# Performance work log

Hardware: AMD Instinct MI355X
Metric: run time of the kernel (lower is better)

The kernel has to match this reference:

```python
import jax, jax.numpy as jnp
import numpy as np

TEMP = 0.07
BASE_TEMP = 0.07
NUM_CLASSES = 1000


def setup_inputs() -> dict:
    key = jax.random.key(0)
    k1, k2, k3, k4 = jax.random.split(key, 4)
    B, V, D, Q = 1024, 2, 128, 65536
    features = jax.random.normal(k1, (B, V, D), jnp.float32)
    features = features / jnp.linalg.norm(features, axis=-1, keepdims=True)
    labels = jax.random.randint(k2, (B,), 0, NUM_CLASSES)
    queue = jax.random.normal(k3, (Q, D), jnp.float32)
    queue = queue / jnp.linalg.norm(queue, axis=-1, keepdims=True)
    queue_labels = jax.random.randint(k4, (Q,), 0, NUM_CLASSES)
    return {"features": features, "labels": labels, "queue": queue, "queue_labels": queue_labels}


def reference(features, labels, queue, queue_labels):
    # features: [B, 2, D]; queue: [Q, D]; labels: [B]; queue_labels: [Q]
    B = features.shape[0]
    f1 = features[:, 0]  # view 1 -> enqueued at the front of the queue
    f2 = features[:, 1]  # view 2 -> anchor
    queue_new = jnp.concatenate([f1, queue[:-B]], axis=0)            # [Q, D]
    qlab_new = jnp.concatenate([labels, queue_labels[:-B]], axis=0)  # [Q]

    # anchor_dot_contrast: [B, Q]
    logits = jnp.matmul(f2, queue_new.T) / TEMP
    logits = logits - jax.lax.stop_gradient(jnp.max(logits, axis=1, keepdims=True))

    rows = jnp.arange(B)
    # scatter(ones, 1, arange(B).view(-1,1), 0): zero at (i, i) -> excludes own enqueued view
    self_mask = jnp.ones(logits.shape, logits.dtype).at[rows, rows].set(0.0)
    pos_mask = (labels[:, None] == qlab_new[None, :]).astype(logits.dtype)  # [B, Q]
    neg_mask = jnp.square(pos_mask - 1.0)  # 1 where different class (pre self-mask), else 0
    pos_mask = pos_mask * self_mask

    e = jnp.exp(logits)
    # supervised term: denominator over negatives only
    log_prob = logits - jnp.log(jnp.sum(e * neg_mask, axis=1, keepdims=True))
    mean_log_prob_pos = jnp.sum(pos_mask * log_prob, axis=1) / jnp.sum(pos_mask, axis=1)

    # triplet/self term: denominator over everything except the self column
    log_self_diff = logits - jnp.log(jnp.sum(e * self_mask, axis=1, keepdims=True))
    triplet = log_self_diff[rows, rows]  # sim_mask selects the paired-view column (i, i)

    scale = TEMP / BASE_TEMP
    loss = jnp.mean(-scale * (triplet + mean_log_prob_pos) / 2.0)
    self_loss = jnp.mean(-scale * triplet)
    class_loss = jnp.mean(-scale * mean_log_prob_pos)
    return (loss, self_loss, class_loss)
```

## Files before the change

kernel.cpp:

```cpp
#include <hip/hip_runtime.h>
#include <math.h>

#define BB 1024
#define DD 128
#define QQ 65536
#define CHUNK 32
#define THREADS 256
#define COLS_PER_BLOCK 128
#define F2G (BB / COLS_PER_BLOCK)
#define NSLICES 256
#define INV_T 14.285714285714286f
#define SCALE 20.609929155556627f
#define LN2F 0.6931471805599453f

typedef short short8 __attribute__((ext_vector_type(8)));
typedef float f32x4  __attribute__((ext_vector_type(4)));
typedef unsigned short us4 __attribute__((ext_vector_type(4)));

#if __has_builtin(__builtin_amdgcn_exp2f)
#define EXP2F(x) __builtin_amdgcn_exp2f(x)
#else
#define EXP2F(x) exp2f(x)
#endif

static __device__ __forceinline__ unsigned short bf16rne(float f) {
    union { float f; unsigned u; } v; v.f = f;
    unsigned r = (v.u + 0x7FFFu + ((v.u >> 16) & 1u)) >> 16;
    return (unsigned short)r;
}

static __device__ __forceinline__ short8 pack8s(float4 x, float4 y) {
    short8 r;
    r[0]=(short)bf16rne(x.x*SCALE); r[1]=(short)bf16rne(x.y*SCALE);
    r[2]=(short)bf16rne(x.z*SCALE); r[3]=(short)bf16rne(x.w*SCALE);
    r[4]=(short)bf16rne(y.x*SCALE); r[5]=(short)bf16rne(y.y*SCALE);
    r[6]=(short)bf16rne(y.z*SCALE); r[7]=(short)bf16rne(y.w*SCALE);
    return r;
}
static __device__ __forceinline__ short8 pack8(float4 x, float4 y) {
    short8 r;
    r[0]=(short)bf16rne(x.x); r[1]=(short)bf16rne(x.y);
    r[2]=(short)bf16rne(x.z); r[3]=(short)bf16rne(x.w);
    r[4]=(short)bf16rne(y.x); r[5]=(short)bf16rne(y.y);
    r[6]=(short)bf16rne(y.z); r[7]=(short)bf16rne(y.w);
    return r;
}

template<int PREK>
__global__ __launch_bounds__(256)
void k1_conv(const float* __restrict__ features, const int* __restrict__ labels,
             const float* __restrict__ queue, const int* __restrict__ queue_labels,
             unsigned short* __restrict__ qbf, int* __restrict__ qlabn,
             unsigned short* __restrict__ f2bf, float* __restrict__ srr)
{
    const int blk = blockIdx.x;
    const int t = blk * 256 + threadIdx.x;
    if (PREK && blk < 512) {
        if (blk < 256)
            qlabn[t] = (t < BB) ? labels[t] : queue_labels[t - BB];
#pragma unroll
        for (int k = 0; k < 16; ++k) {
            int u = k * 131072 + t;
            int e = u * 4;
            int row = e >> 7;
            const float* src = (row < BB) ? (features + (size_t)row * 2 * DD + (e & 127))
                                          : (queue + ((size_t)e - (size_t)BB * DD));
            float4 v = *reinterpret_cast<const float4*>(src);
            us4 pk;
            pk[0] = bf16rne(v.x); pk[1] = bf16rne(v.y);
            pk[2] = bf16rne(v.z); pk[3] = bf16rne(v.w);
            *reinterpret_cast<us4*>(qbf + (size_t)e) = pk;
        }
    } else {
        int r = (PREK ? (blk - 512) : blk) * 256 + threadIdx.x;
        const float* f2p = features + (size_t)r * 2 * DD + DD;
        const float* f1p = features + (size_t)r * 2 * DD;
        float d = 0.f;
#pragma unroll
        for (int k = 0; k < DD / 8; ++k) {
            float4 a0 = reinterpret_cast<const float4*>(f2p)[2 * k];
            float4 a1 = reinterpret_cast<const float4*>(f2p)[2 * k + 1];
            float4 b0 = reinterpret_cast<const float4*>(f1p)[2 * k];
            float4 b1 = reinterpret_cast<const float4*>(f1p)[2 * k + 1];
            d += a0.x * b0.x + a0.y * b0.y + a0.z * b0.z + a0.w * b0.w;
            d += a1.x * b1.x + a1.y * b1.y + a1.z * b1.z + a1.w * b1.w;
            if (PREK)
                *reinterpret_cast<short8*>(f2bf + (size_t)r * DD + k * 8) = pack8s(a0, a1);
        }
        srr[r] = d;
    }
}

template<int PRE>
__global__ __launch_bounds__(THREADS)
void supcon_main(const float* __restrict__ features, const int* __restrict__ labels,
                 const float* __restrict__ queue, const int* __restrict__ queue_labels,
                 const unsigned short* __restrict__ qbf, const int* __restrict__ qlabn,
                 const unsigned short* __restrict__ f2bf,
                 float* __restrict__ stats, int nslices)
{
    __shared__ int4 ldsbuf[2][512];

    const int tid = threadIdx.x;
    const int l = tid & 63, w = tid >> 6;
    const int bid = blockIdx.x;
    const int slice = bid % nslices, f2g = bid / nslices;
    const int sliceRows = QQ / nslices;
    const int nchunks = sliceRows / CHUNK;
    const int colbase = f2g * COLS_PER_BLOCK + w * 32;

    short8 bf[2][4];
    int mylab[2];
#pragma unroll
    for (int b = 0; b < 2; ++b) {
        int r = colbase + b * 16 + (l & 15);
        mylab[b] = labels[r];
        if (PRE) {
            const unsigned short* fp = f2bf + (size_t)r * DD + ((l >> 4) * 8);
#pragma unroll
            for (int kk = 0; kk < 4; ++kk)
                bf[b][kk] = *reinterpret_cast<const short8*>(fp + kk * 32);
        } else {
            const float* fp = features + (size_t)r * 2 * DD + DD + ((l >> 4) * 8);
#pragma unroll
            for (int kk = 0; kk < 4; ++kk) {
                float4 x = *reinterpret_cast<const float4*>(fp + kk * 32);
                float4 y = *reinterpret_cast<const float4*>(fp + kk * 32 + 4);
                bf[b][kk] = pack8s(x, y);
            }
        }
    }

    float tot[2]  = {0.f,0.f};
    float pose[2] = {0.f,0.f};
    float psum[2] = {0.f,0.f};
    float npos[2] = {0.f,0.f};

    const int srow = tid >> 3, sseg = tid & 7;
    const int swzs = (srow & 7) << 4;
    const int j0base = slice * sliceRows;

    {
        int j = j0base + srow;
        char* base = (char*)&ldsbuf[0][0] + srow * 256;
        int cb0 = (sseg * 32) ^ swzs;
        if (PRE) {
            const short8* src = reinterpret_cast<const short8*>(
                qbf + (size_t)j * DD + sseg * 16);
            *reinterpret_cast<short8*>(base + cb0)        = src[0];
            *reinterpret_cast<short8*>(base + (cb0 ^ 16)) = src[1];
        } else {
            const float* src = ((j < BB) ? (features + (size_t)j * 2 * DD)
                                         : (queue + (size_t)(j - BB) * DD)) + sseg * 16;
            float4 p0 = reinterpret_cast<const float4*>(src)[0];
            float4 p1 = reinterpret_cast<const float4*>(src)[1];
            float4 p2 = reinterpret_cast<const float4*>(src)[2];
            float4 p3 = reinterpret_cast<const float4*>(src)[3];
            *reinterpret_cast<short8*>(base + cb0)        = pack8(p0, p1);
            *reinterpret_cast<short8*>(base + (cb0 ^ 16)) = pack8(p2, p3);
        }
    }

    int cur = 0;
    for (int c = 0; c < nchunks; ++c) {
        __syncthreads();
        const int cj0 = j0base + c * CHUNK;
        const bool havenext = (c + 1 < nchunks);

        short8 nlo, nhi;
        float4 p0, p1, p2, p3;
        if (havenext) {
            int j = cj0 + CHUNK + srow;
            if (PRE) {
                const short8* src = reinterpret_cast<const short8*>(
                    qbf + (size_t)j * DD + sseg * 16);
                nlo = src[0]; nhi = src[1];
            } else {
                const float* src = ((j < BB) ? (features + (size_t)j * 2 * DD)
                                             : (queue + (size_t)(j - BB) * DD)) + sseg * 16;
                p0 = reinterpret_cast<const float4*>(src)[0];
                p1 = reinterpret_cast<const float4*>(src)[1];
                p2 = reinterpret_cast<const float4*>(src)[2];
                p3 = reinterpret_cast<const float4*>(src)[3];
            }
        }

        const char* abase = (const char*)&ldsbuf[cur][0];
#pragma unroll
        for (int t2 = 0; t2 < 2; ++t2) {
            const int row = t2 * 16 + (l & 15);
            const char* rbase = abase + row * 256;
            const int g16 = (l >> 4) * 16;
            const int swz = (row & 7) << 4;
            const int j0 = cj0 + t2 * 16 + ((l >> 4) << 2);

            int4 ql4;
            if (PRE) ql4 = *reinterpret_cast<const int4*>(qlabn + j0);
            else ql4 = (j0 < BB) ? *reinterpret_cast<const int4*>(labels + j0)
                                 : *reinterpret_cast<const int4*>(queue_labels + (j0 - BB));
            const int* ql = reinterpret_cast<const int*>(&ql4);

            f32x4 acc[2];
#pragma unroll
            for (int b = 0; b < 2; ++b) acc[b] = f32x4{0.f,0.f,0.f,0.f};
#pragma unroll
            for (int kk = 0; kk < 4; ++kk) {
                short8 a = *reinterpret_cast<const short8*>(rbase + ((kk * 64 + g16) ^ swz));
#pragma unroll
                for (int b = 0; b < 2; ++b)
                    acc[b] = __builtin_amdgcn_mfma_f32_16x16x32_bf16(a, bf[b][kk], acc[b], 0, 0, 0);
            }
#pragma unroll
            for (int b = 0; b < 2; ++b) {
#pragma unroll
                for (int reg = 0; reg < 4; ++reg) {
                    float a = acc[b][reg];
                    float e = EXP2F(a);
                    float pf = (ql[reg] == mylab[b]) ? 1.0f : 0.0f;
                    tot[b]  += e;
                    pose[b]  = fmaf(pf, e, pose[b]);
                    psum[b]  = fmaf(pf, a, psum[b]);
                    npos[b] += pf;
                }
            }
        }

        if (havenext) {
            char* base = (char*)&ldsbuf[cur ^ 1][0] + srow * 256;
            int cb0 = (sseg * 32) ^ swzs;
            if (PRE) {
                *reinterpret_cast<short8*>(base + cb0)        = nlo;
                *reinterpret_cast<short8*>(base + (cb0 ^ 16)) = nhi;
            } else {
                *reinterpret_cast<short8*>(base + cb0)        = pack8(p0, p1);
                *reinterpret_cast<short8*>(base + (cb0 ^ 16)) = pack8(p2, p3);
            }
            cur ^= 1;
        }
    }

#pragma unroll
    for (int b = 0; b < 2; ++b) {
#pragma unroll
        for (int off = 16; off <= 32; off <<= 1) {
            tot[b]  += __shfl_xor(tot[b],  off);
            pose[b] += __shfl_xor(pose[b], off);
            psum[b] += __shfl_xor(psum[b], off);
            npos[b] += __shfl_xor(npos[b], off);
        }
    }
    if ((l >> 4) == 0) {
#pragma unroll
        for (int b = 0; b < 2; ++b) {
            float4 v; v.x = tot[b]; v.y = pose[b]; v.z = psum[b]; v.w = npos[b];
            *reinterpret_cast<float4*>(
                stats + ((size_t)(colbase + b * 16 + l) * nslices + slice) * 4) = v;
        }
    }
}

__global__ __launch_bounds__(256)
void f1_rows(const float* __restrict__ stats, const float* __restrict__ srr,
             float* __restrict__ partials, int nslices)
{
    __shared__ float red[4][2];
    int wv = threadIdx.x >> 6, lane = threadIdx.x & 63;
    int r = blockIdx.x * 4 + wv;
    float tot = 0.f, pose = 0.f, ps = 0.f, np = 0.f;
    for (int s = lane; s < nslices; s += 64) {
        float4 v = reinterpret_cast<const float4*>(stats)[(size_t)r * nslices + s];
        tot += v.x; pose += v.y; ps += v.z; np += v.w;
    }
#pragma unroll
    for (int off = 32; off > 0; off >>= 1) {
        tot  += __shfl_xor(tot,  off);
        pose += __shfl_xor(pose, off);
        ps   += __shfl_xor(ps,   off);
        np   += __shfl_xor(np,   off);
    }
    if (lane == 0) {
        float neg  = tot - pose;
        float srow = srr[r] * INV_T;
        float trip = srow - logf(tot - expf(srow));
        float w    = 1.f / (np - 1.f);
        float mlpp = (ps * LN2F - srow) * w - logf(neg);
        red[wv][0] = trip; red[wv][1] = mlpp;
    }
    __syncthreads();
    if (threadIdx.x == 0) {
        partials[blockIdx.x * 2]     = red[0][0] + red[1][0] + red[2][0] + red[3][0];
        partials[blockIdx.x * 2 + 1] = red[0][1] + red[1][1] + red[2][1] + red[3][1];
    }
}

__global__ __launch_bounds__(256)
void f2_out(const float* __restrict__ partials, float* __restrict__ out)
{
    __shared__ float red[4][2];
    int wv = threadIdx.x >> 6, lane = threadIdx.x & 63;
    float2 v = reinterpret_cast<const float2*>(partials)[threadIdx.x];
    float a = v.x, b = v.y;
#pragma unroll
    for (int off = 32; off > 0; off >>= 1) {
        a += __shfl_xor(a, off);
        b += __shfl_xor(b, off);
    }
    if (lane == 0) { red[wv][0] = a; red[wv][1] = b; }
    __syncthreads();
    if (threadIdx.x == 0) {
        float aT = red[0][0] + red[1][0] + red[2][0] + red[3][0];
        float aM = red[0][1] + red[1][1] + red[2][1] + red[3][1];
        float selfl  = -aT / (float)BB;
        float classl = -aM / (float)BB;
        out[0] = 0.5f * (selfl + classl);
        out[1] = selfl;
        out[2] = classl;
    }
}

extern "C" void kernel_launch(void* const* d_in, const int* in_sizes, int n_in,
                              void* d_out, int out_size, void* d_ws, size_t ws_size,
                              hipStream_t stream)
{
    const float* features     = (const float*)d_in[0];
    const int*   labels       = (const int*)  d_in[1];
    const float* queue        = (const float*)d_in[2];
    const int*   queue_labels = (const int*)  d_in[3];
    char* ws = (char*)d_ws;

    const size_t qbf_sz      = (size_t)QQ * DD * 2;
    const size_t f2bf_sz     = (size_t)BB * DD * 2;
    const size_t qlabn_sz    = (size_t)QQ * 4;
    const size_t srr_sz      = 4096;
    const size_t partials_sz = 2048;

    int nslices = NSLICES;
    size_t stats_sz = (size_t)BB * nslices * 16;
    bool pre = ws_size >= qbf_sz + f2bf_sz + qlabn_sz + stats_sz + srr_sz + partials_sz;
    if (!pre) {
        while ((size_t)BB * nslices * 16 + srr_sz + partials_sz > ws_size && nslices > 8)
            nslices >>= 1;
        stats_sz = (size_t)BB * nslices * 16;
    }

    size_t off = 0;
    unsigned short* qbf = nullptr; unsigned short* f2bf = nullptr; int* qlabn = nullptr;
    if (pre) {
        qbf   = (unsigned short*)(ws + off); off += qbf_sz;
        f2bf  = (unsigned short*)(ws + off); off += f2bf_sz;
        qlabn = (int*)(ws + off);            off += qlabn_sz;
    }
    float* stats    = (float*)(ws + off); off += stats_sz;
    float* srr      = (float*)(ws + off); off += srr_sz;
    float* partials = (float*)(ws + off); off += partials_sz;

    if (pre) {
        k1_conv<1><<<dim3(516), dim3(256), 0, stream>>>(
            features, labels, queue, queue_labels, qbf, qlabn, f2bf, srr);
        supcon_main<1><<<dim3(F2G * nslices), dim3(THREADS), 0, stream>>>(
            features, labels, queue, queue_labels, qbf, qlabn, f2bf, stats, nslices);
    } else {
        k1_conv<0><<<dim3(4), dim3(256), 0, stream>>>(
            features, labels, queue, queue_labels, nullptr, nullptr, nullptr, srr);
        supcon_main<0><<<dim3(F2G * nslices), dim3(THREADS), 0, stream>>>(
            features, labels, queue, queue_labels, nullptr, nullptr, nullptr, stats, nslices);
    }

    f1_rows<<<dim3(BB / 4), dim3(256), 0, stream>>>(stats, srr, partials, nslices);
    f2_out<<<dim3(1), dim3(256), 0, stream>>>(partials, (float*)d_out);
}
```

Measured before the change: 63.29 us.

## Drop bf16 pre-conversion kernel and convert fp32 inputs on the fly

Removes the k1_conv pre-pass that converted the whole queue to bf16 in workspace along with the pre-scaled f2 copy and the concatenated labels. The main kernel now always reads fp32 features and queue and packs them to bf16 inline while staging into LDS. The self-similarity dot product moves into f1_rows. This saves one launch and a 16MB bf16 write, but the main kernel now reads twice the bytes per queue row (fp32 instead of bf16) and the f2 bf16 packing is redone in every block.

```diff
diff --git a/kernel.cpp b/kernel.cpp
--- a/kernel.cpp
+++ b/kernel.cpp
@@ -15,7 +15,6 @@
 
 typedef short short8 __attribute__((ext_vector_type(8)));
 typedef float f32x4  __attribute__((ext_vector_type(4)));
-typedef unsigned short us4 __attribute__((ext_vector_type(4)));
 
 #if __has_builtin(__builtin_amdgcn_exp2f)
 #define EXP2F(x) __builtin_amdgcn_exp2f(x)
@@ -46,57 +45,9 @@
     return r;
 }
 
-template<int PREK>
-__global__ __launch_bounds__(256)
-void k1_conv(const float* __restrict__ features, const int* __restrict__ labels,
-             const float* __restrict__ queue, const int* __restrict__ queue_labels,
-             unsigned short* __restrict__ qbf, int* __restrict__ qlabn,
-             unsigned short* __restrict__ f2bf, float* __restrict__ srr)
-{
-    const int blk = blockIdx.x;
-    const int t = blk * 256 + threadIdx.x;
-    if (PREK && blk < 512) {
-        if (blk < 256)
-            qlabn[t] = (t < BB) ? labels[t] : queue_labels[t - BB];
-#pragma unroll
-        for (int k = 0; k < 16; ++k) {
-            int u = k * 131072 + t;
-            int e = u * 4;
-            int row = e >> 7;
-            const float* src = (row < BB) ? (features + (size_t)row * 2 * DD + (e & 127))
-                                          : (queue + ((size_t)e - (size_t)BB * DD));
-            float4 v = *reinterpret_cast<const float4*>(src);
-            us4 pk;
-            pk[0] = bf16rne(v.x); pk[1] = bf16rne(v.y);
-            pk[2] = bf16rne(v.z); pk[3] = bf16rne(v.w);
-            *reinterpret_cast<us4*>(qbf + (size_t)e) = pk;
-        }
-    } else {
-        int r = (PREK ? (blk - 512) : blk) * 256 + threadIdx.x;
-        const float* f2p = features + (size_t)r * 2 * DD + DD;
-        const float* f1p = features + (size_t)r * 2 * DD;
-        float d = 0.f;
-#pragma unroll
-        for (int k = 0; k < DD / 8; ++k) {
-            float4 a0 = reinterpret_cast<const float4*>(f2p)[2 * k];
-            float4 a1 = reinterpret_cast<const float4*>(f2p)[2 * k + 1];
-            float4 b0 = reinterpret_cast<const float4*>(f1p)[2 * k];
-            float4 b1 = reinterpret_cast<const float4*>(f1p)[2 * k + 1];
-            d += a0.x * b0.x + a0.y * b0.y + a0.z * b0.z + a0.w * b0.w;
-            d += a1.x * b1.x + a1.y * b1.y + a1.z * b1.z + a1.w * b1.w;
-            if (PREK)
-                *reinterpret_cast<short8*>(f2bf + (size_t)r * DD + k * 8) = pack8s(a0, a1);
-        }
-        srr[r] = d;
-    }
-}
-
-template<int PRE>
 __global__ __launch_bounds__(THREADS)
 void supcon_main(const float* __restrict__ features, const int* __restrict__ labels,
                  const float* __restrict__ queue, const int* __restrict__ queue_labels,
-                 const unsigned short* __restrict__ qbf, const int* __restrict__ qlabn,
-                 const unsigned short* __restrict__ f2bf,
                  float* __restrict__ stats, int nslices)
 {
     __shared__ int4 ldsbuf[2][512];
@@ -115,19 +66,12 @@
     for (int b = 0; b < 2; ++b) {
         int r = colbase + b * 16 + (l & 15);
         mylab[b] = labels[r];
-        if (PRE) {
-            const unsigned short* fp = f2bf + (size_t)r * DD + ((l >> 4) * 8);
-#pragma unroll
-            for (int kk = 0; kk < 4; ++kk)
-                bf[b][kk] = *reinterpret_cast<const short8*>(fp + kk * 32);
-        } else {
-            const float* fp = features + (size_t)r * 2 * DD + DD + ((l >> 4) * 8);
-#pragma unroll
-            for (int kk = 0; kk < 4; ++kk) {
-                float4 x = *reinterpret_cast<const float4*>(fp + kk * 32);
-                float4 y = *reinterpret_cast<const float4*>(fp + kk * 32 + 4);
-                bf[b][kk] = pack8s(x, y);
-            }
+        const float* fp = features + (size_t)r * 2 * DD + DD + ((l >> 4) * 8);
+#pragma unroll
+        for (int kk = 0; kk < 4; ++kk) {
+            float4 x = *reinterpret_cast<const float4*>(fp + kk * 32);
+            float4 y = *reinterpret_cast<const float4*>(fp + kk * 32 + 4);
+            bf[b][kk] = pack8s(x, y);
         }
     }
 
@@ -142,23 +86,16 @@
 
     {
         int j = j0base + srow;
+        const float* src = ((j < BB) ? (features + (size_t)j * 2 * DD)
+                                     : (queue + (size_t)(j - BB) * DD)) + sseg * 16;
+        float4 p0 = reinterpret_cast<const float4*>(src)[0];
+        float4 p1 = reinterpret_cast<const float4*>(src)[1];
+        float4 p2 = reinterpret_cast<const float4*>(src)[2];
+        float4 p3 = reinterpret_cast<const float4*>(src)[3];
         char* base = (char*)&ldsbuf[0][0] + srow * 256;
         int cb0 = (sseg * 32) ^ swzs;
-        if (PRE) {
-            const short8* src = reinterpret_cast<const short8*>(
-                qbf + (size_t)j * DD + sseg * 16);
-            *reinterpret_cast<short8*>(base + cb0)        = src[0];
-            *reinterpret_cast<short8*>(base + (cb0 ^ 16)) = src[1];
-        } else {
-            const float* src = ((j < BB) ? (features + (size_t)j * 2 * DD)
-                                         : (queue + (size_t)(j - BB) * DD)) + sseg * 16;
-            float4 p0 = reinterpret_cast<const float4*>(src)[0];
-            float4 p1 = reinterpret_cast<const float4*>(src)[1];
-            float4 p2 = reinterpret_cast<const float4*>(src)[2];
-            float4 p3 = reinterpret_cast<const float4*>(src)[3];
-            *reinterpret_cast<short8*>(base + cb0)        = pack8(p0, p1);
-            *reinterpret_cast<short8*>(base + (cb0 ^ 16)) = pack8(p2, p3);
-        }
+        *reinterpret_cast<short8*>(base + cb0)        = pack8(p0, p1);
+        *reinterpret_cast<short8*>(base + (cb0 ^ 16)) = pack8(p2, p3);
     }
 
     int cur = 0;
@@ -167,22 +104,15 @@
         const int cj0 = j0base + c * CHUNK;
         const bool havenext = (c + 1 < nchunks);
 
-        short8 nlo, nhi;
         float4 p0, p1, p2, p3;
         if (havenext) {
             int j = cj0 + CHUNK + srow;
-            if (PRE) {
-                const short8* src = reinterpret_cast<const short8*>(
-                    qbf + (size_t)j * DD + sseg * 16);
-                nlo = src[0]; nhi = src[1];
-            } else {
-                const float* src = ((j < BB) ? (features + (size_t)j * 2 * DD)
-                                             : (queue + (size_t)(j - BB) * DD)) + sseg * 16;
-                p0 = reinterpret_cast<const float4*>(src)[0];
-                p1 = reinterpret_cast<const float4*>(src)[1];
-                p2 = reinterpret_cast<const float4*>(src)[2];
-                p3 = reinterpret_cast<const float4*>(src)[3];
-            }
+            const float* src = ((j < BB) ? (features + (size_t)j * 2 * DD)
+                                         : (queue + (size_t)(j - BB) * DD)) + sseg * 16;
+            p0 = reinterpret_cast<const float4*>(src)[0];
+            p1 = reinterpret_cast<const float4*>(src)[1];
+            p2 = reinterpret_cast<const float4*>(src)[2];
+            p3 = reinterpret_cast<const float4*>(src)[3];
         }
 
         const char* abase = (const char*)&ldsbuf[cur][0];
@@ -194,9 +124,7 @@
             const int swz = (row & 7) << 4;
             const int j0 = cj0 + t2 * 16 + ((l >> 4) << 2);
 
-            int4 ql4;
-            if (PRE) ql4 = *reinterpret_cast<const int4*>(qlabn + j0);
-            else ql4 = (j0 < BB) ? *reinterpret_cast<const int4*>(labels + j0)
+            int4 ql4 = (j0 < BB) ? *reinterpret_cast<const int4*>(labels + j0)
                                  : *reinterpret_cast<const int4*>(queue_labels + (j0 - BB));
             const int* ql = reinterpret_cast<const int*>(&ql4);
 
@@ -228,13 +156,8 @@
         if (havenext) {
             char* base = (char*)&ldsbuf[cur ^ 1][0] + srow * 256;
             int cb0 = (sseg * 32) ^ swzs;
-            if (PRE) {
-                *reinterpret_cast<short8*>(base + cb0)        = nlo;
-                *reinterpret_cast<short8*>(base + (cb0 ^ 16)) = nhi;
-            } else {
-                *reinterpret_cast<short8*>(base + cb0)        = pack8(p0, p1);
-                *reinterpret_cast<short8*>(base + (cb0 ^ 16)) = pack8(p2, p3);
-            }
+            *reinterpret_cast<short8*>(base + cb0)        = pack8(p0, p1);
+            *reinterpret_cast<short8*>(base + (cb0 ^ 16)) = pack8(p2, p3);
             cur ^= 1;
         }
     }
@@ -260,7 +183,7 @@
 }
 
 __global__ __launch_bounds__(256)
-void f1_rows(const float* __restrict__ stats, const float* __restrict__ srr,
+void f1_rows(const float* __restrict__ stats, const float* __restrict__ features,
              float* __restrict__ partials, int nslices)
 {
     __shared__ float red[4][2];
@@ -271,19 +194,24 @@
         float4 v = reinterpret_cast<const float4*>(stats)[(size_t)r * nslices + s];
         tot += v.x; pose += v.y; ps += v.z; np += v.w;
     }
+    const float* fr = features + (size_t)r * 2 * DD;
+    float2 vb = reinterpret_cast<const float2*>(fr)[lane];
+    float2 va = reinterpret_cast<const float2*>(fr + DD)[lane];
+    float d = va.x * vb.x + va.y * vb.y;
 #pragma unroll
     for (int off = 32; off > 0; off >>= 1) {
         tot  += __shfl_xor(tot,  off);
         pose += __shfl_xor(pose, off);
         ps   += __shfl_xor(ps,   off);
         np   += __shfl_xor(np,   off);
+        d    += __shfl_xor(d,    off);
     }
     if (lane == 0) {
         float neg  = tot - pose;
-        float srow = srr[r] * INV_T;
+        float srow = d * INV_T;
         float trip = srow - logf(tot - expf(srow));
-        float w    = 1.f / (np - 1.f);
-        float mlpp = (ps * LN2F - srow) * w - logf(neg);
+        float wgt  = 1.f / (np - 1.f);
+        float mlpp = (ps * LN2F - srow) * wgt - logf(neg);
         red[wv][0] = trip; red[wv][1] = mlpp;
     }
     __syncthreads();
@@ -328,44 +256,17 @@
     const int*   queue_labels = (const int*)  d_in[3];
     char* ws = (char*)d_ws;
 
-    const size_t qbf_sz      = (size_t)QQ * DD * 2;
-    const size_t f2bf_sz     = (size_t)BB * DD * 2;
-    const size_t qlabn_sz    = (size_t)QQ * 4;
-    const size_t srr_sz      = 4096;
     const size_t partials_sz = 2048;
-
     int nslices = NSLICES;
+    while ((size_t)BB * nslices * 16 + partials_sz > ws_size && nslices > 8)
+        nslices >>= 1;
     size_t stats_sz = (size_t)BB * nslices * 16;
-    bool pre = ws_size >= qbf_sz + f2bf_sz + qlabn_sz + stats_sz + srr_sz + partials_sz;
-    if (!pre) {
-        while ((size_t)BB * nslices * 16 + srr_sz + partials_sz > ws_size && nslices > 8)
-            nslices >>= 1;
-        stats_sz = (size_t)BB * nslices * 16;
-    }
-
-    size_t off = 0;
-    unsigned short* qbf = nullptr; unsigned short* f2bf = nullptr; int* qlabn = nullptr;
-    if (pre) {
-        qbf   = (unsigned short*)(ws + off); off += qbf_sz;
-        f2bf  = (unsigned short*)(ws + off); off += f2bf_sz;
-        qlabn = (int*)(ws + off);            off += qlabn_sz;
-    }
-    float* stats    = (float*)(ws + off); off += stats_sz;
-    float* srr      = (float*)(ws + off); off += srr_sz;
-    float* partials = (float*)(ws + off); off += partials_sz;
-
-    if (pre) {
-        k1_conv<1><<<dim3(516), dim3(256), 0, stream>>>(
-            features, labels, queue, queue_labels, qbf, qlabn, f2bf, srr);
-        supcon_main<1><<<dim3(F2G * nslices), dim3(THREADS), 0, stream>>>(
-            features, labels, queue, queue_labels, qbf, qlabn, f2bf, stats, nslices);
-    } else {
-        k1_conv<0><<<dim3(4), dim3(256), 0, stream>>>(
-            features, labels, queue, queue_labels, nullptr, nullptr, nullptr, srr);
-        supcon_main<0><<<dim3(F2G * nslices), dim3(THREADS), 0, stream>>>(
-            features, labels, queue, queue_labels, nullptr, nullptr, nullptr, stats, nslices);
-    }
-
-    f1_rows<<<dim3(BB / 4), dim3(256), 0, stream>>>(stats, srr, partials, nslices);
+
+    float* stats    = (float*)ws;
+    float* partials = (float*)(ws + stats_sz);
+
+    supcon_main<<<dim3(F2G * nslices), dim3(THREADS), 0, stream>>>(
+        features, labels, queue, queue_labels, stats, nslices);
+    f1_rows<<<dim3(BB / 4), dim3(256), 0, stream>>>(stats, features, partials, nslices);
     f2_out<<<dim3(1), dim3(256), 0, stream>>>(partials, (float*)d_out);
 }
```

Result: faster. 57.45 us (-9.2%).
